# Kernel tuning notes

Hardware: AMD Instinct MI355X
Metric: run time of the kernel (lower is better)

Reference implementation:

```python
import jax, jax.numpy as jnp
import numpy as np

B, S, H, NH = 2, 2048, 2048, 16
HD = H // NH


def setup_inputs() -> dict:
    key = jax.random.key(0)
    ks = jax.random.split(key, 9)
    s = 1.0 / np.sqrt(H)
    return {
        "hidden_state": jax.random.normal(ks[0], (B, S, H), dtype=jnp.float32),
        "Wq": jax.random.normal(ks[1], (H, H), dtype=jnp.float32) * s,
        "bq": jnp.zeros((H,), dtype=jnp.float32),
        "Wk": jax.random.normal(ks[2], (H, H), dtype=jnp.float32) * s,
        "bk": jnp.zeros((H,), dtype=jnp.float32),
        "Wv": jax.random.normal(ks[3], (H, H), dtype=jnp.float32) * s,
        "bv": jnp.zeros((H,), dtype=jnp.float32),
        "Wo": jax.random.normal(ks[4], (H, H), dtype=jnp.float32) * s,
        "bo": jnp.zeros((H,), dtype=jnp.float32),
    }


def _split_heads(x):
    # [B,S,H] -> [B,NH,S,HD]
    b, s, _ = x.shape
    return x.reshape(b, s, NH, HD).transpose(0, 2, 1, 3)


def reference(hidden_state, Wq, bq, Wk, bk, Wv, bv, Wo, bo):
    q = _split_heads(hidden_state @ Wq.T + bq)
    k = _split_heads(hidden_state @ Wk.T + bk)
    v = _split_heads(hidden_state @ Wv.T + bv)
    scale = 1.0 / jnp.sqrt(jnp.array(HD, dtype=q.dtype))
    scores = jnp.einsum("bhqd,bhkd->bhqk", q, k) * scale
    attn = jax.nn.softmax(scores, axis=-1)
    out = jnp.einsum("bhqk,bhkd->bhqd", attn, v)  # [B,NH,S,HD]
    out = out.transpose(0, 2, 1, 3).reshape(hidden_state.shape[0], -1, H)
    return out @ Wo.T + bo
```

## Files before the change

### kernel.cpp

```cpp
#include <hip/hip_runtime.h>
#include <hip/hip_bf16.h>
#include <stdint.h>

#define B_ 2
#define S_ 2048
#define H_ 2048
#define NH_ 16
#define HD_ 128
#define M_ (B_*S_)

typedef __attribute__((ext_vector_type(8))) short short8_t;
typedef __attribute__((ext_vector_type(4))) float floatx4;

__device__ __forceinline__ short f2bf(float f) {
  union { float f; uint32_t u; } x; x.f = f;
  const uint32_t u = x.u;
  return (short)((u + 0x7FFFu + ((u >> 16) & 1u)) >> 16);
}

__device__ __forceinline__ void gload_lds16(const void* g, void* l) {
  __builtin_amdgcn_global_load_lds(
      (const __attribute__((address_space(1))) void*)g,
      (__attribute__((address_space(3))) void*)l, 16, 0, 0);
}

__global__ __launch_bounds__(256)
void cast_all(const float* __restrict__ h,  const float* __restrict__ wq,
              const float* __restrict__ wk, const float* __restrict__ wv,
              const float* __restrict__ wo,
              short* __restrict__ hB,  short* __restrict__ wqB,
              short* __restrict__ wkB, short* __restrict__ wvB,
              short* __restrict__ woB) {
  const int blk = blockIdx.x;
  const float* src; short* dst; int off;
  if      (blk <  4096) { src = h;  dst = hB;  off = blk; }
  else if (blk <  6144) { src = wq; dst = wqB; off = blk - 4096; }
  else if (blk <  8192) { src = wk; dst = wkB; off = blk - 6144; }
  else if (blk < 10240) { src = wv; dst = wvB; off = blk - 8192; }
  else                  { src = wo; dst = woB; off = blk - 10240; }
  const int i = (off * 256 + threadIdx.x) * 8;
  typedef __attribute__((ext_vector_type(4))) float f4;
  const f4 a = *(const f4*)(src + i);
  const f4 b = *(const f4*)(src + i + 4);
  short8_t o;
  o[0] = f2bf(a[0]); o[1] = f2bf(a[1]); o[2] = f2bf(a[2]); o[3] = f2bf(a[3]);
  o[4] = f2bf(b[0]); o[5] = f2bf(b[1]); o[6] = f2bf(b[2]); o[7] = f2bf(b[3]);
  *(short8_t*)(dst + i) = o;
}

template<int MODE>
__device__ __forceinline__
void gemm_body(const short* __restrict__ A, const short* __restrict__ Bm,
               const float* __restrict__ bias, void* __restrict__ C,
               const int m0, const int n0, const int N, const int K) {
  __shared__ short As[128 * 32];
  __shared__ short Bs[128 * 32];
  const int tid = threadIdx.x;
  const int wv = tid >> 6, ln = tid & 63;
  const int lr = ln >> 4, lc = ln & 15;
  const int wm = (wv >> 1) * 64, wn = (wv & 1) * 64;
  const int srow = ln >> 2, sch = (ln & 3) * 8;

  floatx4 acc[4][4] = {};
  const short* aBase = A  + (size_t)(m0 + srow) * K + sch;
  const short* bBase = Bm + (size_t)(n0 + srow) * K + sch;

  for (int k0 = 0; k0 < K; k0 += 32) {
#pragma unroll
    for (int inst = 0; inst < 2; ++inst) {
      const int rb = inst * 64 + wv * 16;
      gload_lds16(aBase + (size_t)rb * K + k0, &As[rb * 32]);
      gload_lds16(bBase + (size_t)rb * K + k0, &Bs[rb * 32]);
    }
    __syncthreads();
    short8_t af[4], bf[4];
#pragma unroll
    for (int t = 0; t < 4; ++t)
      af[t] = *(const short8_t*)&As[(wm + t * 16 + lc) * 32 + lr * 8];
#pragma unroll
    for (int t = 0; t < 4; ++t)
      bf[t] = *(const short8_t*)&Bs[(wn + t * 16 + lc) * 32 + lr * 8];
#pragma unroll
    for (int i = 0; i < 4; ++i)
#pragma unroll
      for (int j = 0; j < 4; ++j)
        acc[i][j] = __builtin_amdgcn_mfma_f32_16x16x32_bf16(af[i], bf[j], acc[i][j], 0, 0, 0);
    __syncthreads();
  }

#pragma unroll
  for (int i = 0; i < 4; ++i) {
#pragma unroll
    for (int j = 0; j < 4; ++j) {
      const int col = n0 + wn + j * 16 + lc;
      const float bv = bias[col];
#pragma unroll
      for (int r = 0; r < 4; ++r) {
        const int row = m0 + wm + i * 16 + lr * 4 + r;
        const float v = acc[i][j][r] + bv;
        if (MODE == 1) {
          ((float*)C)[(size_t)row * N + col] = v;
        } else if (MODE == 0) {
          ((short*)C)[(size_t)row * N + col] = f2bf(v);
        } else {
          const int bb = row >> 11, s = row & 2047;
          const int kt = s >> 6, key = s & 63;
          const int hh = col >> 7, d = col & 127;
          const int cp = d ^ ((key & 7) << 3);
          ((short*)C)[((((size_t)(bb * 16 + hh) * 32 + kt) * 64 + key) << 7) + cp] = f2bf(v);
        }
      }
    }
  }
}

__global__ __launch_bounds__(256)
void gemm_qkv(const short* __restrict__ A,
              const short* __restrict__ W0, const short* __restrict__ W1, const short* __restrict__ W2,
              const float* __restrict__ b0, const float* __restrict__ b1, const float* __restrict__ b2,
              short* __restrict__ C0, short* __restrict__ C1, short* __restrict__ C2) {
  const int sel = blockIdx.x >> 4;
  const int n0 = (blockIdx.x & 15) * 128, m0 = blockIdx.y * 128;
  if (sel == 0)      gemm_body<0>(A, W0, b0, C0, m0, n0, H_, H_);
  else if (sel == 1) gemm_body<2>(A, W1, b1, C1, m0, n0, H_, H_);
  else               gemm_body<0>(A, W2, b2, C2, m0, n0, H_, H_);
}

__global__ __launch_bounds__(256)
void gemm_out(const short* __restrict__ A, const short* __restrict__ Bm,
              const float* __restrict__ bias, float* __restrict__ C) {
  gemm_body<1>(A, Bm, bias, C, blockIdx.y * 128, blockIdx.x * 128, H_, H_);
}

__global__ __launch_bounds__(256)
void arrange_v(const short* __restrict__ V, short* __restrict__ Vt) {
  __shared__ short T[64][72];
  const int b = blockIdx.z;
  const int s0 = blockIdx.x * 64, c0 = blockIdx.y * 64;
  const int t = threadIdx.x;
  const int r = t >> 3, c8 = (t & 7) * 8;
  const int kt = s0 >> 6;
#pragma unroll
  for (int p = 0; p < 2; ++p) {
    const int row = p * 32 + r;
    *(short8_t*)&T[row][c8] =
        *(const short8_t*)&V[(size_t)(b * S_ + s0 + row) * H_ + c0 + c8];
  }
  __syncthreads();
#pragma unroll
  for (int p = 0; p < 2; ++p) {
    const int row = p * 32 + r;
    const int gcol = c0 + row;
    const int hh = gcol >> 7, d = gcol & 127;
    short8_t o;
#pragma unroll
    for (int j = 0; j < 8; ++j) o[j] = T[c8 + j][row];
    const int chunk = (c8 >> 3) ^ (d & 7);
    *(short8_t*)&Vt[((((size_t)(b * 16 + hh) * 32 + kt) * 128 + d) << 6) + chunk * 8] = o;
  }
}

__global__ __launch_bounds__(512, 4)
void attention(const short* __restrict__ Q, const short* __restrict__ Kt,
               const short* __restrict__ Vt, short* __restrict__ O) {
  __shared__ short Ks[64 * 128];
  __shared__ short Vs[128 * 64];
  __shared__ short Ps[128 * 64];

  const int tid = threadIdx.x;
  const int wv = tid >> 6, ln = tid & 63;
  const int lr = ln >> 4, lc = ln & 15;
  const int bh = blockIdx.y, b = bh >> 4, h = bh & 15;
  const int qw = blockIdx.x * 128 + wv * 16;

  const short* Qp  = Q  + ((size_t)(b * S_ + qw)) * H_ + h * HD_;
  const short* KtB = Kt + (size_t)bh * (S_ * HD_);
  const short* VtB = Vt + (size_t)bh * (S_ * HD_);

  short8_t qf[4];
#pragma unroll
  for (int ksq = 0; ksq < 4; ++ksq)
    qf[ksq] = *(const short8_t*)&Qp[(size_t)lc * H_ + ksq * 32 + lr * 8];

  floatx4 oacc[8] = {};
  float lsum[4] = {};
  const float csc = 0.08838834764831845f * 1.4426950408889634f;
  const int sA = (lc & 7) << 3;
  const int i0 = wv * 1024 + ln * 8;

  for (int kt = 0; kt < S_ / 64; ++kt) {
    const size_t tb = (size_t)kt * 8192;
    gload_lds16(KtB + tb + i0,       &Ks[wv * 1024]);
    gload_lds16(KtB + tb + i0 + 512, &Ks[wv * 1024 + 512]);
    gload_lds16(VtB + tb + i0,       &Vs[wv * 1024]);
    gload_lds16(VtB + tb + i0 + 512, &Vs[wv * 1024 + 512]);
    __syncthreads();

    floatx4 sacc[4] = {};
#pragma unroll
    for (int ksq = 0; ksq < 4; ++ksq) {
#pragma unroll
      for (int tj = 0; tj < 4; ++tj) {
        const short8_t kf =
            *(const short8_t*)&Ks[(tj * 16 + lc) * 128 + ((ksq * 32 + lr * 8) ^ sA)];
        sacc[tj] = __builtin_amdgcn_mfma_f32_16x16x32_bf16(qf[ksq], kf, sacc[tj], 0, 0, 0);
      }
    }

#pragma unroll
    for (int tj = 0; tj < 4; ++tj) {
#pragma unroll
      for (int r = 0; r < 4; ++r) {
        const float p = exp2f(sacc[tj][r] * csc);
        const uint32_t u = __float_as_uint(p);
        const int row = wv * 16 + lr * 4 + r;
        Ps[row * 64 + ((tj * 16 + lc) ^ ((row & 7) << 3))] = (short)(u >> 16);
        lsum[r] += __uint_as_float(u & 0xffff0000u);
      }
    }

#pragma unroll
    for (int ks = 0; ks < 2; ++ks) {
      const short8_t pf =
          *(const short8_t*)&Ps[(wv * 16 + lc) * 64 + ((ks * 32 + lr * 8) ^ sA)];
#pragma unroll
      for (int tj = 0; tj < 8; ++tj) {
        const short8_t vf =
            *(const short8_t*)&Vs[(tj * 16 + lc) * 64 + ((ks * 32 + lr * 8) ^ sA)];
        oacc[tj] = __builtin_amdgcn_mfma_f32_16x16x32_bf16(pf, vf, oacc[tj], 0, 0, 0);
      }
    }
    __syncthreads();
  }

  short* Op = O + ((size_t)(b * S_ + qw)) * H_ + h * HD_;
#pragma unroll
  for (int r = 0; r < 4; ++r) {
    float l = lsum[r];
    l += __shfl_xor(l, 1);
    l += __shfl_xor(l, 2);
    l += __shfl_xor(l, 4);
    l += __shfl_xor(l, 8);
    const float inv = 1.0f / l;
#pragma unroll
    for (int tj = 0; tj < 8; ++tj)
      Op[(size_t)(lr * 4 + r) * H_ + tj * 16 + lc] = f2bf(oacc[tj][r] * inv);
  }
}

extern "C" void kernel_launch(void* const* d_in, const int* in_sizes, int n_in,
                              void* d_out, int out_size, void* d_ws, size_t ws_size,
                              hipStream_t stream) {
  const float* hidden = (const float*)d_in[0];
  const float* Wq = (const float*)d_in[1];
  const float* bq = (const float*)d_in[2];
  const float* Wk = (const float*)d_in[3];
  const float* bk = (const float*)d_in[4];
  const float* Wv = (const float*)d_in[5];
  const float* bv = (const float*)d_in[6];
  const float* Wo = (const float*)d_in[7];
  const float* bo = (const float*)d_in[8];
  float* out = (float*)d_out;

  char* ws = (char*)d_ws;
  short* hB  = (short*)(ws);
  short* WqB = (short*)(ws + (16u << 20));
  short* WkB = (short*)(ws + (24u << 20));
  short* WvB = (short*)(ws + (32u << 20));
  short* WoB = (short*)(ws + (40u << 20));
  short* Qb  = (short*)(ws + (48u << 20));
  short* Ktb = (short*)(ws + (64u << 20));
  short* Vb  = (short*)(ws + (80u << 20));
  short* Vtb = (short*)(ws + (96u << 20));
  short* Ob  = (short*)(ws + (112u << 20));

  cast_all<<<12288, 256, 0, stream>>>(hidden, Wq, Wk, Wv, Wo, hB, WqB, WkB, WvB, WoB);

  gemm_qkv<<<dim3(48, M_ / 128), 256, 0, stream>>>(hB, WqB, WkB, WvB, bq, bk, bv, Qb, Ktb, Vb);

  arrange_v<<<dim3(S_ / 64, H_ / 64, B_), 256, 0, stream>>>(Vb, Vtb);

  attention<<<dim3(S_ / 128, B_ * NH_), 512, 0, stream>>>(Qb, Ktb, Vtb, Ob);

  gemm_out<<<dim3(H_ / 128, M_ / 128), 256, 0, stream>>>(Ob, WoB, bo, out);
}
```

Measured before the change: 428.9 us.

## Deepen GEMM K-tile with swizzled LDS, gather K directly, coalesce attention output

The GEMM body now loads 64-wide K slices per iteration into XOR-swizzled LDS, halving barrier count, and is templated on M tile so the output projection uses 64-row tiles for more blocks. The QKV GEMM no longer writes K in a scattered pre-tiled layout; attention instead loads K rows straight from the row-major buffer with a swizzled global_load_lds pattern. The attention epilogue stages the output through LDS to issue 16-byte coalesced stores instead of scalar 2-byte stores. These target LDS bank conflicts, scattered epilogue writes and low occupancy in the output GEMM, at the cost of more LDS per block and extra sync.

```diff
diff --git a/kernel.cpp b/kernel.cpp
--- a/kernel.cpp
+++ b/kernel.cpp
@@ -48,48 +48,61 @@
   *(short8_t*)(dst + i) = o;
 }
 
-template<int MODE>
+template<int MT, int MODE>
 __device__ __forceinline__
 void gemm_body(const short* __restrict__ A, const short* __restrict__ Bm,
                const float* __restrict__ bias, void* __restrict__ C,
                const int m0, const int n0, const int N, const int K) {
-  __shared__ short As[128 * 32];
-  __shared__ short Bs[128 * 32];
+  constexpr int MI = MT / 32;
+  __shared__ short As[MT * 64];
+  __shared__ short Bs[128 * 64];
   const int tid = threadIdx.x;
   const int wv = tid >> 6, ln = tid & 63;
   const int lr = ln >> 4, lc = ln & 15;
-  const int wm = (wv >> 1) * 64, wn = (wv & 1) * 64;
-  const int srow = ln >> 2, sch = (ln & 3) * 8;
-
-  floatx4 acc[4][4] = {};
-  const short* aBase = A  + (size_t)(m0 + srow) * K + sch;
-  const short* bBase = Bm + (size_t)(n0 + srow) * K + sch;
-
-  for (int k0 = 0; k0 < K; k0 += 32) {
-#pragma unroll
-    for (int inst = 0; inst < 2; ++inst) {
-      const int rb = inst * 64 + wv * 16;
-      gload_lds16(aBase + (size_t)rb * K + k0, &As[rb * 32]);
-      gload_lds16(bBase + (size_t)rb * K + k0, &Bs[rb * 32]);
-    }
+  const int wm = (wv >> 1) * (MT / 2);
+  const int wn = (wv & 1) * 64;
+  const int srow = ln >> 3;
+  const int sc   = (ln & 7) ^ srow;
+
+  floatx4 acc[MI][4] = {};
+  const short* aP[MT / 32];
+  const short* bP[4];
+#pragma unroll
+  for (int i = 0; i < MT / 32; ++i)
+    aP[i] = A + (size_t)(m0 + wv * (MT / 4) + i * 8 + srow) * K + sc * 8;
+#pragma unroll
+  for (int i = 0; i < 4; ++i)
+    bP[i] = Bm + (size_t)(n0 + wv * 32 + i * 8 + srow) * K + sc * 8;
+  const int sw = (lc & 7) << 3;
+
+  for (int k0 = 0; k0 < K; k0 += 64) {
+#pragma unroll
+    for (int i = 0; i < MT / 32; ++i)
+      gload_lds16(aP[i] + k0, &As[(wv * (MT / 4) + i * 8) * 64]);
+#pragma unroll
+    for (int i = 0; i < 4; ++i)
+      gload_lds16(bP[i] + k0, &Bs[(wv * 32 + i * 8) * 64]);
     __syncthreads();
-    short8_t af[4], bf[4];
-#pragma unroll
-    for (int t = 0; t < 4; ++t)
-      af[t] = *(const short8_t*)&As[(wm + t * 16 + lc) * 32 + lr * 8];
-#pragma unroll
-    for (int t = 0; t < 4; ++t)
-      bf[t] = *(const short8_t*)&Bs[(wn + t * 16 + lc) * 32 + lr * 8];
-#pragma unroll
-    for (int i = 0; i < 4; ++i)
-#pragma unroll
-      for (int j = 0; j < 4; ++j)
-        acc[i][j] = __builtin_amdgcn_mfma_f32_16x16x32_bf16(af[i], bf[j], acc[i][j], 0, 0, 0);
+#pragma unroll
+    for (int ksq = 0; ksq < 2; ++ksq) {
+      short8_t af[MI], bf[4];
+#pragma unroll
+      for (int t = 0; t < MI; ++t)
+        af[t] = *(const short8_t*)&As[(wm + t * 16 + lc) * 64 + ((ksq * 32 + lr * 8) ^ sw)];
+#pragma unroll
+      for (int t = 0; t < 4; ++t)
+        bf[t] = *(const short8_t*)&Bs[(wn + t * 16 + lc) * 64 + ((ksq * 32 + lr * 8) ^ sw)];
+#pragma unroll
+      for (int i = 0; i < MI; ++i)
+#pragma unroll
+        for (int j = 0; j < 4; ++j)
+          acc[i][j] = __builtin_amdgcn_mfma_f32_16x16x32_bf16(af[i], bf[j], acc[i][j], 0, 0, 0);
+    }
     __syncthreads();
   }
 
 #pragma unroll
-  for (int i = 0; i < 4; ++i) {
+  for (int i = 0; i < MI; ++i) {
 #pragma unroll
     for (int j = 0; j < 4; ++j) {
       const int col = n0 + wn + j * 16 + lc;
@@ -98,17 +111,8 @@
       for (int r = 0; r < 4; ++r) {
         const int row = m0 + wm + i * 16 + lr * 4 + r;
         const float v = acc[i][j][r] + bv;
-        if (MODE == 1) {
-          ((float*)C)[(size_t)row * N + col] = v;
-        } else if (MODE == 0) {
-          ((short*)C)[(size_t)row * N + col] = f2bf(v);
-        } else {
-          const int bb = row >> 11, s = row & 2047;
-          const int kt = s >> 6, key = s & 63;
-          const int hh = col >> 7, d = col & 127;
-          const int cp = d ^ ((key & 7) << 3);
-          ((short*)C)[((((size_t)(bb * 16 + hh) * 32 + kt) * 64 + key) << 7) + cp] = f2bf(v);
-        }
+        if (MODE == 1) ((float*)C)[(size_t)row * N + col] = v;
+        else           ((short*)C)[(size_t)row * N + col] = f2bf(v);
       }
     }
   }
@@ -120,16 +124,16 @@
               const float* __restrict__ b0, const float* __restrict__ b1, const float* __restrict__ b2,
               short* __restrict__ C0, short* __restrict__ C1, short* __restrict__ C2) {
   const int sel = blockIdx.x >> 4;
-  const int n0 = (blockIdx.x & 15) * 128, m0 = blockIdx.y * 128;
-  if (sel == 0)      gemm_body<0>(A, W0, b0, C0, m0, n0, H_, H_);
-  else if (sel == 1) gemm_body<2>(A, W1, b1, C1, m0, n0, H_, H_);
-  else               gemm_body<0>(A, W2, b2, C2, m0, n0, H_, H_);
+  const short* Bm   = sel == 0 ? W0 : (sel == 1 ? W1 : W2);
+  const float* bias = sel == 0 ? b0 : (sel == 1 ? b1 : b2);
+  short* C          = sel == 0 ? C0 : (sel == 1 ? C1 : C2);
+  gemm_body<128, 0>(A, Bm, bias, C, blockIdx.y * 128, (blockIdx.x & 15) * 128, H_, H_);
 }
 
 __global__ __launch_bounds__(256)
 void gemm_out(const short* __restrict__ A, const short* __restrict__ Bm,
               const float* __restrict__ bias, float* __restrict__ C) {
-  gemm_body<1>(A, Bm, bias, C, blockIdx.y * 128, blockIdx.x * 128, H_, H_);
+  gemm_body<64, 1>(A, Bm, bias, C, blockIdx.y * 64, blockIdx.x * 128, H_, H_);
 }
 
 __global__ __launch_bounds__(256)
@@ -161,7 +165,7 @@
 }
 
 __global__ __launch_bounds__(512, 4)
-void attention(const short* __restrict__ Q, const short* __restrict__ Kt,
+void attention(const short* __restrict__ Q, const short* __restrict__ Kg,
                const short* __restrict__ Vt, short* __restrict__ O) {
   __shared__ short Ks[64 * 128];
   __shared__ short Vs[128 * 64];
@@ -174,8 +178,12 @@
   const int qw = blockIdx.x * 128 + wv * 16;
 
   const short* Qp  = Q  + ((size_t)(b * S_ + qw)) * H_ + h * HD_;
-  const short* KtB = Kt + (size_t)bh * (S_ * HD_);
   const short* VtB = Vt + (size_t)bh * (S_ * HD_);
+
+  const int kl0 = ln >> 4,        c0_ = (ln & 15) ^ (kl0 & 7);
+  const int kl1 = 4 + (ln >> 4),  c1_ = (ln & 15) ^ (kl1 & 7);
+  const short* kp0 = Kg + ((size_t)(b * S_ + wv * 8 + kl0) * H_ + h * HD_ + c0_ * 8);
+  const short* kp1 = Kg + ((size_t)(b * S_ + wv * 8 + kl1) * H_ + h * HD_ + c1_ * 8);
 
   short8_t qf[4];
 #pragma unroll
@@ -189,9 +197,10 @@
   const int i0 = wv * 1024 + ln * 8;
 
   for (int kt = 0; kt < S_ / 64; ++kt) {
+    const size_t kadv = (size_t)kt * 64 * H_;
     const size_t tb = (size_t)kt * 8192;
-    gload_lds16(KtB + tb + i0,       &Ks[wv * 1024]);
-    gload_lds16(KtB + tb + i0 + 512, &Ks[wv * 1024 + 512]);
+    gload_lds16(kp0 + kadv,          &Ks[(wv * 8) * 128]);
+    gload_lds16(kp1 + kadv,          &Ks[(wv * 8 + 4) * 128]);
     gload_lds16(VtB + tb + i0,       &Vs[wv * 1024]);
     gload_lds16(VtB + tb + i0 + 512, &Vs[wv * 1024 + 512]);
     __syncthreads();
@@ -233,7 +242,7 @@
     __syncthreads();
   }
 
-  short* Op = O + ((size_t)(b * S_ + qw)) * H_ + h * HD_;
+  float inv[4];
 #pragma unroll
   for (int r = 0; r < 4; ++r) {
     float l = lsum[r];
@@ -241,10 +250,26 @@
     l += __shfl_xor(l, 2);
     l += __shfl_xor(l, 4);
     l += __shfl_xor(l, 8);
-    const float inv = 1.0f / l;
-#pragma unroll
-    for (int tj = 0; tj < 8; ++tj)
-      Op[(size_t)(lr * 4 + r) * H_ + tj * 16 + lc] = f2bf(oacc[tj][r] * inv);
+    inv[r] = 1.0f / l;
+  }
+  __syncthreads();
+  short* Kw = &Ks[wv * 1024];
+  short* Op = O + ((size_t)(b * S_ + qw)) * H_ + h * HD_;
+  const int orow = ln >> 2, ocp = (ln & 3) * 2;
+#pragma unroll
+  for (int hh = 0; hh < 2; ++hh) {
+#pragma unroll
+    for (int tj = 0; tj < 4; ++tj)
+#pragma unroll
+      for (int r = 0; r < 4; ++r) {
+        const int row = lr * 4 + r;
+        Kw[row * 64 + ((tj * 16 + lc) ^ ((row & 7) << 3))] =
+            f2bf(oacc[hh * 4 + tj][r] * inv[r]);
+      }
+    const short8_t v0 = *(const short8_t*)&Kw[orow * 64 + ((ocp * 8) ^ ((orow & 7) << 3))];
+    const short8_t v1 = *(const short8_t*)&Kw[orow * 64 + (((ocp + 1) * 8) ^ ((orow & 7) << 3))];
+    *(short8_t*)&Op[(size_t)orow * H_ + hh * 64 + ocp * 8]     = v0;
+    *(short8_t*)&Op[(size_t)orow * H_ + hh * 64 + ocp * 8 + 8] = v1;
   }
 }
 
@@ -269,18 +294,18 @@
   short* WvB = (short*)(ws + (32u << 20));
   short* WoB = (short*)(ws + (40u << 20));
   short* Qb  = (short*)(ws + (48u << 20));
-  short* Ktb = (short*)(ws + (64u << 20));
+  short* Kb  = (short*)(ws + (64u << 20));
   short* Vb  = (short*)(ws + (80u << 20));
   short* Vtb = (short*)(ws + (96u << 20));
   short* Ob  = (short*)(ws + (112u << 20));
 
   cast_all<<<12288, 256, 0, stream>>>(hidden, Wq, Wk, Wv, Wo, hB, WqB, WkB, WvB, WoB);
 
-  gemm_qkv<<<dim3(48, M_ / 128), 256, 0, stream>>>(hB, WqB, WkB, WvB, bq, bk, bv, Qb, Ktb, Vb);
+  gemm_qkv<<<dim3(48, M_ / 128), 256, 0, stream>>>(hB, WqB, WkB, WvB, bq, bk, bv, Qb, Kb, Vb);
 
   arrange_v<<<dim3(S_ / 64, H_ / 64, B_), 256, 0, stream>>>(Vb, Vtb);
 
-  attention<<<dim3(S_ / 128, B_ * NH_), 512, 0, stream>>>(Qb, Ktb, Vtb, Ob);
-
-  gemm_out<<<dim3(H_ / 128, M_ / 128), 256, 0, stream>>>(Ob, WoB, bo, out);
-}
+  attention<<<dim3(S_ / 128, B_ * NH_), 512, 0, stream>>>(Qb, Kb, Vtb, Ob);
+
+  gemm_out<<<dim3(H_ / 128, M_ / 64), 256, 0, stream>>>(Ob, WoB, bo, out);
+}
```

Result: no change. 424.3 us (-1.1%).
